# Optimization experiments

Measured on AMD Instinct MI355X. Metric: run time of the kernel, lower is better.

Reference implementation:

```python
import jax, jax.numpy as jnp
import numpy as np
import math

EMBED_DIM = 512
NUM_CLASSES = 100000
BATCH = 1024
MARGIN = 0.5
SCALE = 64.0


def setup_inputs() -> dict:
    key = jax.random.key(0)
    k1, k2, k3 = jax.random.split(key, 3)
    embeddings = jax.random.normal(k1, (BATCH, EMBED_DIM), dtype=jnp.float32)
    labels = jax.random.randint(k2, (BATCH,), 0, NUM_CLASSES, dtype=jnp.int64)
    # xavier_uniform for weight [num_classes, embedding_dim]
    limit = math.sqrt(6.0 / (NUM_CLASSES + EMBED_DIM))
    weight = jax.random.uniform(k3, (NUM_CLASSES, EMBED_DIM), dtype=jnp.float32,
                                minval=-limit, maxval=limit)
    return {"embeddings": embeddings, "weight": weight, "labels": labels}


def _l2norm(x, axis=-1, eps=1e-12):
    # matches torch F.normalize (p=2, eps=1e-12)
    n = jnp.linalg.norm(x, axis=axis, keepdims=True)
    return x / jnp.maximum(n, eps)


def reference(embeddings, weight, labels):
    cos_m = math.cos(MARGIN)
    sin_m = math.sin(MARGIN)
    th = math.cos(math.pi - MARGIN)
    mm = math.sin(math.pi - MARGIN) * MARGIN

    # cosine similarity: [B, C]
    cosine = _l2norm(embeddings) @ _l2norm(weight).T
    sine = jnp.sqrt(jnp.clip(1.0 - cosine * cosine, 0.0, 1.0))
    phi = cosine * cos_m - sine * sin_m
    phi = jnp.where(cosine > th, phi, cosine - mm)

    # apply margin only at the label position
    one_hot = jax.nn.one_hot(labels, NUM_CLASSES, dtype=cosine.dtype)
    logits = SCALE * (one_hot * phi + (1.0 - one_hot) * cosine)

    # cross entropy, mean reduction
    logp = jax.nn.log_softmax(logits, axis=-1)
    nll = -jnp.take_along_axis(logp, labels[:, None], axis=1)[:, 0]
    return jnp.mean(nll)
```

## Files before the change

### kernel.cpp

```cpp
#include <hip/hip_runtime.h>
#include <hip/hip_bf16.h>
#include <math.h>

#define B_ROWS 1024
#define EMB    512
#define NCLS   100000
#define SCALE_ 64.0f
#define COS_M 0.8775825618903728f
#define SIN_M 0.479425538604203f
#define TH_C  (-0.8775825618903728f)
#define MM_C  0.2397127693021015f

#define BM 128
#define BN 128
#define BK 32
#define NTILES 782
#define KCHUNKS 16

typedef __attribute__((ext_vector_type(8))) short bf16x8;
typedef __attribute__((ext_vector_type(4))) float f32x4;

typedef __attribute__((address_space(1))) const unsigned int GLP;
typedef __attribute__((address_space(3))) unsigned int LDP;

__device__ __forceinline__ float bf2f(short u) {
  unsigned int x = ((unsigned int)(unsigned short)u) << 16;
  return __builtin_bit_cast(float, x);
}
__device__ __forceinline__ short f2bf(float f) {
  unsigned int u = __builtin_bit_cast(unsigned int, f);
  u += 0x7FFF + ((u >> 16) & 1);
  return (short)(u >> 16);
}

__device__ __forceinline__ void load16(const void* g, void* l) {
  __builtin_amdgcn_global_load_lds((GLP*)g, (LDP*)l, 16, 0, 0);
}

__global__ void setup_kernel(const void* __restrict__ emb, const int* __restrict__ labels,
                             float* __restrict__ row_sum, float* __restrict__ accum,
                             int* __restrict__ flag, int* __restrict__ dflag) {
  const int t = threadIdx.x;
  row_sum[t] = 0.f;
  row_sum[t + 512] = 0.f;
  if (t == 0) *accum = 0.f;

  if (t < 64) {
    bf16x8 v = *(const bf16x8*)((const short*)emb + t * 8);
    float s = 0.f;
    #pragma unroll
    for (int j = 0; j < 8; ++j) { float f = bf2f(v[j]); s += f * f; }
    #pragma unroll
    for (int off = 1; off < 64; off <<= 1) s += __shfl_xor(s, off);
    if (t == 0) *dflag = (s < 1e8f) ? 1 : 0;
  }

  int v = labels[2 * t + 1];
  #pragma unroll
  for (int off = 1; off < 64; off <<= 1) v |= __shfl_xor(v, off);
  __shared__ int red[8];
  if ((t & 63) == 0) red[t >> 6] = v;
  __syncthreads();
  if (t == 0) {
    int o = 0;
    #pragma unroll
    for (int i = 0; i < 8; ++i) o |= red[i];
    *flag = (o == 0) ? 1 : 0;
  }
}

__global__ void normconv_kernel(const void* __restrict__ emb, const void* __restrict__ wgt,
                                const int* __restrict__ dflag,
                                float* __restrict__ inv_e, float* __restrict__ inv_w,
                                short* __restrict__ An, short* __restrict__ Wn,
                                const int do_conv) {
  const int wave = threadIdx.x >> 6;
  const int lane = threadIdx.x & 63;
  const int row = blockIdx.x * 4 + wave;
  int r;
  const void* base;
  float* dst;
  short* out;
  if (row < B_ROWS) { r = row; base = emb; dst = inv_e + row; out = An + (size_t)row * EMB; }
  else {
    r = row - B_ROWS;
    if (r >= NCLS) return;
    base = wgt; dst = inv_w + r; out = Wn + (size_t)r * EMB;
  }
  float f[8];
  if (*dflag) {
    const short* p = (const short*)base + (size_t)r * EMB;
    bf16x8 v = *(const bf16x8*)(p + lane * 8);
    #pragma unroll
    for (int j = 0; j < 8; ++j) f[j] = bf2f(v[j]);
  } else {
    const float* p = (const float*)base + (size_t)r * EMB;
    f32x4 x = *(const f32x4*)(p + lane * 8);
    f32x4 y = *(const f32x4*)(p + lane * 8 + 4);
    #pragma unroll
    for (int j = 0; j < 4; ++j) { f[j] = x[j]; f[j + 4] = y[j]; }
  }
  float s = 0.f;
  #pragma unroll
  for (int j = 0; j < 8; ++j) s += f[j] * f[j];
  #pragma unroll
  for (int off = 1; off < 64; off <<= 1) s += __shfl_xor(s, off);
  const float inv = 1.f / fmaxf(sqrtf(s), 1e-12f);
  if (lane == 0) *dst = inv;
  if (do_conv) {
    bf16x8 o;
    #pragma unroll
    for (int j = 0; j < 8; ++j) o[j] = f2bf(f[j] * inv);
    *(bf16x8*)(out + lane * 8) = o;
  }
}

__global__ __launch_bounds__(256, 3) void arc_gemm_fast(
    const short* __restrict__ A, const short* __restrict__ W,
    const int* __restrict__ labels, const int* __restrict__ flag,
    float* __restrict__ row_sum, float* __restrict__ lablogit) {
  __shared__ short As[BM * BK];
  __shared__ short Bs[BN * BK];
  __shared__ int   sh_lab[BM];
  __shared__ float sh_sum[BM][2];

  const int tid  = threadIdx.x;
  const int wave = tid >> 6;
  const int lane = tid & 63;
  const int wy = wave >> 1;
  const int wx = wave & 1;
  const int lr = lane & 15;
  const int lk = lane >> 4;
  const int mBase = blockIdx.x * BM;
  const int nBase = blockIdx.y * BN;

  const int srow  = lane >> 2;
  const int sbyte = (lane & 3) * 16;

  f32x4 zero = {0.f, 0.f, 0.f, 0.f};
  f32x4 acc[4][4];
  #pragma unroll
  for (int i = 0; i < 4; ++i)
    #pragma unroll
    for (int j = 0; j < 4; ++j) acc[i][j] = zero;

  const char* Ab = (const char*)A;
  const char* Wb = (const char*)W;

  for (int kc = 0; kc < KCHUNKS; ++kc) {
    __syncthreads();
    const size_t koff = (size_t)kc * 64 + sbyte;
    #pragma unroll
    for (int it = 0; it < 2; ++it) {
      const int c = wave + it * 4;
      const int ar = mBase + c * 16 + srow;
      load16(Ab + (size_t)ar * 1024 + koff, (char*)As + (size_t)c * 1024);
      int br = nBase + c * 16 + srow;
      if (br >= NCLS) br = NCLS - 1;
      load16(Wb + (size_t)br * 1024 + koff, (char*)Bs + (size_t)c * 1024);
    }
    __syncthreads();
    bf16x8 af[4], bfr[4];
    #pragma unroll
    for (int mi = 0; mi < 4; ++mi)
      af[mi] = *(const bf16x8*)(As + ((wy * 64 + mi * 16 + lr) * BK + lk * 8));
    #pragma unroll
    for (int ni = 0; ni < 4; ++ni)
      bfr[ni] = *(const bf16x8*)(Bs + ((wx * 64 + ni * 16 + lr) * BK + lk * 8));
    #pragma unroll
    for (int mi = 0; mi < 4; ++mi)
      #pragma unroll
      for (int ni = 0; ni < 4; ++ni)
        acc[mi][ni] = __builtin_amdgcn_mfma_f32_16x16x32_bf16(af[mi], bfr[ni], acc[mi][ni], 0, 0, 0);
  }

  __syncthreads();
  if (tid < BM) {
    const int r = mBase + tid;
    const int f = *flag;
    sh_lab[tid] = labels[f ? (size_t)(2 * r) : (size_t)r];
  }
  __syncthreads();

  #pragma unroll
  for (int mi = 0; mi < 4; ++mi) {
    #pragma unroll
    for (int reg = 0; reg < 4; ++reg) {
      const int lrow = wy * 64 + mi * 16 + lk * 4 + reg;
      const int grow = mBase + lrow;
      const int lab = sh_lab[lrow];
      float s = 0.f;
      #pragma unroll
      for (int ni = 0; ni < 4; ++ni) {
        const int gcol = nBase + wx * 64 + ni * 16 + lr;
        if (gcol < NCLS) {
          const float cosv = acc[mi][ni][reg];
          float logit;
          if (gcol == lab) {
            const float sine = sqrtf(fmaxf(1.f - cosv * cosv, 0.f));
            float phi = cosv * COS_M - sine * SIN_M;
            phi = (cosv > TH_C) ? phi : (cosv - MM_C);
            logit = SCALE_ * phi;
            lablogit[grow] = logit;
          } else {
            logit = SCALE_ * cosv;
          }
          s += __expf(logit - SCALE_);
        }
      }
      #pragma unroll
      for (int off = 1; off < 16; off <<= 1) s += __shfl_xor(s, off);
      if (lr == 0) sh_sum[lrow][wx] = s;
    }
  }
  __syncthreads();
  if (tid < BM)
    atomicAdd(&row_sum[mBase + tid], sh_sum[tid][0] + sh_sum[tid][1]);
}

__global__ __launch_bounds__(256, 3) void arc_gemm(
    const void* __restrict__ A, const void* __restrict__ W,
    const float* __restrict__ inv_e, const float* __restrict__ inv_w,
    const int* __restrict__ labels, const int* __restrict__ flag,
    const int* __restrict__ dflag,
    float* __restrict__ row_sum, float* __restrict__ lablogit) {
  __shared__ short As[BM * BK];
  __shared__ short Bs[BN * BK];
  __shared__ int   sh_lab[BM];
  __shared__ float sh_sum[BM][2];

  const int tid  = threadIdx.x;
  const int wave = tid >> 6;
  const int lane = tid & 63;
  const int wy = wave >> 1;
  const int wx = wave & 1;
  const int lr = lane & 15;
  const int lk = lane >> 4;
  const int mBase = blockIdx.x * BM;
  const int nBase = blockIdx.y * BN;
  const int isbf16 = *dflag;

  const int srow  = lane >> 2;
  const int sbyte = (lane & 3) * 16;

  f32x4 zero = {0.f, 0.f, 0.f, 0.f};
  f32x4 acc[4][4];
  #pragma unroll
  for (int i = 0; i < 4; ++i)
    #pragma unroll
    for (int j = 0; j < 4; ++j) acc[i][j] = zero;

  const char*  Ab = (const char*)A;
  const char*  Wb = (const char*)W;
  const float* Af = (const float*)A;
  const float* Wf = (const float*)W;

  for (int kc = 0; kc < KCHUNKS; ++kc) {
    __syncthreads();
    if (isbf16) {
      const size_t koff = (size_t)kc * 64 + sbyte;
      #pragma unroll
      for (int it = 0; it < 2; ++it) {
        const int c = wave + it * 4;
        const int ar = mBase + c * 16 + srow;
        load16(Ab + (size_t)ar * 1024 + koff, (char*)As + (size_t)c * 1024);
        int br = nBase + c * 16 + srow;
        if (br >= NCLS) br = NCLS - 1;
        load16(Wb + (size_t)br * 1024 + koff, (char*)Bs + (size_t)c * 1024);
      }
    } else {
      #pragma unroll
      for (int p = 0; p < 2; ++p) {
        const int u   = p * 256 + tid;
        const int row = u >> 2;
        const int seg = u & 3;
        const float* ga = Af + ((size_t)(mBase + row) * EMB + kc * 32 + seg * 8);
        f32x4 x = *(const f32x4*)ga;
        f32x4 y = *(const f32x4*)(ga + 4);
        bf16x8 tpack;
        #pragma unroll
        for (int j = 0; j < 4; ++j) { tpack[j] = f2bf(x[j]); tpack[j + 4] = f2bf(y[j]); }
        *(bf16x8*)(As + row * BK + seg * 8) = tpack;
        int br = nBase + row;
        if (br >= NCLS) br = NCLS - 1;
        const float* gb = Wf + ((size_t)br * EMB + kc * 32 + seg * 8);
        x = *(const f32x4*)gb;
        y = *(const f32x4*)(gb + 4);
        #pragma unroll
        for (int j = 0; j < 4; ++j) { tpack[j] = f2bf(x[j]); tpack[j + 4] = f2bf(y[j]); }
        *(bf16x8*)(Bs + row * BK + seg * 8) = tpack;
      }
    }
    __syncthreads();
    bf16x8 af[4], bfr[4];
    #pragma unroll
    for (int mi = 0; mi < 4; ++mi)
      af[mi] = *(const bf16x8*)(As + ((wy * 64 + mi * 16 + lr) * BK + lk * 8));
    #pragma unroll
    for (int ni = 0; ni < 4; ++ni)
      bfr[ni] = *(const bf16x8*)(Bs + ((wx * 64 + ni * 16 + lr) * BK + lk * 8));
    #pragma unroll
    for (int mi = 0; mi < 4; ++mi)
      #pragma unroll
      for (int ni = 0; ni < 4; ++ni)
        acc[mi][ni] = __builtin_amdgcn_mfma_f32_16x16x32_bf16(af[mi], bfr[ni], acc[mi][ni], 0, 0, 0);
  }

  __syncthreads();
  if (tid < BM) {
    const int r = mBase + tid;
    const int f = *flag;
    sh_lab[tid] = labels[f ? (size_t)(2 * r) : (size_t)r];
  }
  __syncthreads();

  #pragma unroll
  for (int mi = 0; mi < 4; ++mi) {
    #pragma unroll
    for (int reg = 0; reg < 4; ++reg) {
      const int lrow = wy * 64 + mi * 16 + lk * 4 + reg;
      const int grow = mBase + lrow;
      const float ie = inv_e[grow];
      const int lab = sh_lab[lrow];
      float s = 0.f;
      #pragma unroll
      for (int ni = 0; ni < 4; ++ni) {
        const int gcol = nBase + wx * 64 + ni * 16 + lr;
        if (gcol < NCLS) {
          const float cosv = acc[mi][ni][reg] * ie * inv_w[gcol];
          float logit;
          if (gcol == lab) {
            const float sine = sqrtf(fmaxf(1.f - cosv * cosv, 0.f));
            float phi = cosv * COS_M - sine * SIN_M;
            phi = (cosv > TH_C) ? phi : (cosv - MM_C);
            logit = SCALE_ * phi;
            lablogit[grow] = logit;
          } else {
            logit = SCALE_ * cosv;
          }
          s += __expf(logit - SCALE_);
        }
      }
      #pragma unroll
      for (int off = 1; off < 16; off <<= 1) s += __shfl_xor(s, off);
      if (lr == 0) sh_sum[lrow][wx] = s;
    }
  }
  __syncthreads();
  if (tid < BM)
    atomicAdd(&row_sum[mBase + tid], sh_sum[tid][0] + sh_sum[tid][1]);
}

__global__ void loss_kernel(const float* __restrict__ row_sum,
                            const float* __restrict__ lablogit,
                            float* __restrict__ accum) {
  const int r = blockIdx.x * 128 + threadIdx.x;
  float loss = SCALE_ + logf(row_sum[r]) - lablogit[r];
  #pragma unroll
  for (int off = 1; off < 64; off <<= 1) loss += __shfl_xor(loss, off);
  __shared__ float rs[2];
  if ((threadIdx.x & 63) == 0) rs[threadIdx.x >> 6] = loss;
  __syncthreads();
  if (threadIdx.x == 0) atomicAdd(accum, rs[0] + rs[1]);
}

__global__ void finalize_kernel(const float* __restrict__ accum, float* __restrict__ out) {
  out[0] = accum[0] * (1.0f / 1024.0f);
}

extern "C" void kernel_launch(void* const* d_in, const int* in_sizes, int n_in,
                              void* d_out, int out_size, void* d_ws, size_t ws_size,
                              hipStream_t stream) {
  const void* emb   = d_in[0];
  const void* wgt   = d_in[1];
  const int* labels = (const int*)d_in[2];
  float* out = (float*)d_out;

  const size_t WN_SHORTS = (size_t)NCLS * EMB;
  const size_t AN_SHORTS = (size_t)B_ROWS * EMB;
  const size_t FAST_NEED = (WN_SHORTS + AN_SHORTS) * 2 + 103075u * 4;

  if (ws_size >= FAST_NEED) {
    short* Wn = (short*)d_ws;
    short* An = Wn + WN_SHORTS;
    float* tail     = (float*)(An + AN_SHORTS);
    float* inv_e    = tail;
    float* inv_w    = tail + 1024;
    float* lablogit = tail + 101024;
    float* row_sum  = tail + 102048;
    float* accum    = tail + 103072;
    int*   flag     = (int*)(tail + 103073);
    int*   dflag    = (int*)(tail + 103074);

    setup_kernel<<<1, 512, 0, stream>>>(emb, labels, row_sum, accum, flag, dflag);
    normconv_kernel<<<(B_ROWS + NCLS) / 4, 256, 0, stream>>>(
        emb, wgt, dflag, inv_e, inv_w, An, Wn, 1);
    dim3 grid(8, NTILES);
    arc_gemm_fast<<<grid, 256, 0, stream>>>(An, Wn, labels, flag, row_sum, lablogit);
    loss_kernel<<<8, 128, 0, stream>>>(row_sum, lablogit, accum);
    finalize_kernel<<<1, 1, 0, stream>>>(accum, out);
  } else {
    float* ws       = (float*)d_ws;
    float* inv_e    = ws;
    float* inv_w    = ws + 1024;
    float* lablogit = ws + 101024;
    float* row_sum  = ws + 102048;
    float* accum    = ws + 103072;
    int*   flag     = (int*)(ws + 103073);
    int*   dflag    = (int*)(ws + 103074);

    setup_kernel<<<1, 512, 0, stream>>>(emb, labels, row_sum, accum, flag, dflag);
    normconv_kernel<<<(B_ROWS + NCLS) / 4, 256, 0, stream>>>(
        emb, wgt, dflag, inv_e, inv_w, (short*)inv_e, (short*)inv_e, 0);
    dim3 grid(8, NTILES);
    arc_gemm<<<grid, 256, 0, stream>>>(emb, wgt, inv_e, inv_w, labels, flag, dflag, row_sum, lablogit);
    loss_kernel<<<8, 128, 0, stream>>>(row_sum, lablogit, accum);
    finalize_kernel<<<1, 1, 0, stream>>>(accum, out);
  }
}
```

Measured before the change: 477.7 us.

## Swizzle LDS layout, remap GEMM tile order, and widen per-thread normalization work

The normalization kernel now gives each row to 16 threads instead of a full wave, so each thread loads and converts more elements with a shorter shuffle reduction. The fast GEMM switches to a 1D grid whose block index is remapped so that 8 consecutive blocks cover different weight tiles grouped for L2 reuse. It also XOR-swizzles the 16-byte chunk positions in the A and B LDS tiles to reduce bank conflicts on MFMA operand reads. The risks are a few idle padded blocks and higher register pressure in the normalization kernel.

Result: faster. 465.3 us (-2.6%).

```diff
diff --git a/kernel.cpp b/kernel.cpp
--- a/kernel.cpp
+++ b/kernel.cpp
@@ -18,6 +18,7 @@
 #define KCHUNKS 16
 
 typedef __attribute__((ext_vector_type(8))) short bf16x8;
+typedef __attribute__((ext_vector_type(4))) short s16x4;
 typedef __attribute__((ext_vector_type(4))) float f32x4;
 
 typedef __attribute__((address_space(1))) const unsigned int GLP;
@@ -69,14 +70,14 @@
   }
 }
 
-__global__ void normconv_kernel(const void* __restrict__ emb, const void* __restrict__ wgt,
-                                const int* __restrict__ dflag,
-                                float* __restrict__ inv_e, float* __restrict__ inv_w,
-                                short* __restrict__ An, short* __restrict__ Wn,
-                                const int do_conv) {
-  const int wave = threadIdx.x >> 6;
-  const int lane = threadIdx.x & 63;
-  const int row = blockIdx.x * 4 + wave;
+__global__ __launch_bounds__(256) void normconv_kernel(
+    const void* __restrict__ emb, const void* __restrict__ wgt,
+    const int* __restrict__ dflag,
+    float* __restrict__ inv_e, float* __restrict__ inv_w,
+    short* __restrict__ An, short* __restrict__ Wn, const int do_conv) {
+  const int sub  = threadIdx.x & 15;
+  const int rloc = threadIdx.x >> 4;
+  const int row  = blockIdx.x * 16 + rloc;
   int r;
   const void* base;
   float* dst;
@@ -87,31 +88,50 @@
     if (r >= NCLS) return;
     base = wgt; dst = inv_w + r; out = Wn + (size_t)r * EMB;
   }
-  float f[8];
-  if (*dflag) {
+  const int isbf16 = *dflag;
+  float f[32];
+  if (isbf16) {
     const short* p = (const short*)base + (size_t)r * EMB;
-    bf16x8 v = *(const bf16x8*)(p + lane * 8);
-    #pragma unroll
-    for (int j = 0; j < 8; ++j) f[j] = bf2f(v[j]);
+    #pragma unroll
+    for (int j = 0; j < 4; ++j) {
+      bf16x8 v = *(const bf16x8*)(p + j * 128 + sub * 8);
+      #pragma unroll
+      for (int t = 0; t < 8; ++t) f[j * 8 + t] = bf2f(v[t]);
+    }
   } else {
     const float* p = (const float*)base + (size_t)r * EMB;
-    f32x4 x = *(const f32x4*)(p + lane * 8);
-    f32x4 y = *(const f32x4*)(p + lane * 8 + 4);
-    #pragma unroll
-    for (int j = 0; j < 4; ++j) { f[j] = x[j]; f[j + 4] = y[j]; }
+    #pragma unroll
+    for (int j = 0; j < 8; ++j) {
+      f32x4 v = *(const f32x4*)(p + j * 64 + sub * 4);
+      #pragma unroll
+      for (int t = 0; t < 4; ++t) f[j * 4 + t] = v[t];
+    }
   }
   float s = 0.f;
   #pragma unroll
-  for (int j = 0; j < 8; ++j) s += f[j] * f[j];
-  #pragma unroll
-  for (int off = 1; off < 64; off <<= 1) s += __shfl_xor(s, off);
+  for (int j = 0; j < 32; ++j) s += f[j] * f[j];
+  #pragma unroll
+  for (int off = 1; off < 16; off <<= 1) s += __shfl_xor(s, off);
   const float inv = 1.f / fmaxf(sqrtf(s), 1e-12f);
-  if (lane == 0) *dst = inv;
+  if (sub == 0) *dst = inv;
   if (do_conv) {
-    bf16x8 o;
-    #pragma unroll
-    for (int j = 0; j < 8; ++j) o[j] = f2bf(f[j] * inv);
-    *(bf16x8*)(out + lane * 8) = o;
+    if (isbf16) {
+      #pragma unroll
+      for (int j = 0; j < 4; ++j) {
+        bf16x8 o;
+        #pragma unroll
+        for (int t = 0; t < 8; ++t) o[t] = f2bf(f[j * 8 + t] * inv);
+        *(bf16x8*)(out + j * 128 + sub * 8) = o;
+      }
+    } else {
+      #pragma unroll
+      for (int j = 0; j < 8; ++j) {
+        s16x4 o;
+        #pragma unroll
+        for (int t = 0; t < 4; ++t) o[t] = f2bf(f[j * 4 + t] * inv);
+        *(s16x4*)(out + j * 64 + sub * 4) = o;
+      }
+    }
   }
 }
 
@@ -119,6 +139,13 @@
     const short* __restrict__ A, const short* __restrict__ W,
     const int* __restrict__ labels, const int* __restrict__ flag,
     float* __restrict__ row_sum, float* __restrict__ lablogit) {
+  const int bid = blockIdx.x;
+  const int k   = bid & 7;
+  const int j   = bid >> 3;
+  const int ytile = (j >> 3) * 8 + k;
+  const int xtile = j & 7;
+  if (ytile >= NTILES) return;
+
   __shared__ short As[BM * BK];
   __shared__ short Bs[BN * BK];
   __shared__ int   sh_lab[BM];
@@ -131,18 +158,19 @@
   const int wx = wave & 1;
   const int lr = lane & 15;
   const int lk = lane >> 4;
-  const int mBase = blockIdx.x * BM;
-  const int nBase = blockIdx.y * BN;
+  const int mBase = xtile * BM;
+  const int nBase = ytile * BN;
 
   const int srow  = lane >> 2;
-  const int sbyte = (lane & 3) * 16;
+  const int sbyte = (((lane & 3) ^ ((lane >> 3) & 3)) << 4);
+  const int rswz  = ((lr >> 1) & 3);
 
   f32x4 zero = {0.f, 0.f, 0.f, 0.f};
   f32x4 acc[4][4];
   #pragma unroll
   for (int i = 0; i < 4; ++i)
     #pragma unroll
-    for (int j = 0; j < 4; ++j) acc[i][j] = zero;
+    for (int jj = 0; jj < 4; ++jj) acc[i][jj] = zero;
 
   const char* Ab = (const char*)A;
   const char* Wb = (const char*)W;
@@ -163,10 +191,10 @@
     bf16x8 af[4], bfr[4];
     #pragma unroll
     for (int mi = 0; mi < 4; ++mi)
-      af[mi] = *(const bf16x8*)(As + ((wy * 64 + mi * 16 + lr) * BK + lk * 8));
+      af[mi] = *(const bf16x8*)(As + ((wy * 64 + mi * 16 + lr) * BK + (lk ^ rswz) * 8));
     #pragma unroll
     for (int ni = 0; ni < 4; ++ni)
-      bfr[ni] = *(const bf16x8*)(Bs + ((wx * 64 + ni * 16 + lr) * BK + lk * 8));
+      bfr[ni] = *(const bf16x8*)(Bs + ((wx * 64 + ni * 16 + lr) * BK + (lk ^ rswz) * 8));
     #pragma unroll
     for (int mi = 0; mi < 4; ++mi)
       #pragma unroll
@@ -376,6 +404,8 @@
   const int* labels = (const int*)d_in[2];
   float* out = (float*)d_out;
 
+  const int NORM_BLOCKS = (B_ROWS + NCLS + 15) / 16;
+
   const size_t WN_SHORTS = (size_t)NCLS * EMB;
   const size_t AN_SHORTS = (size_t)B_ROWS * EMB;
   const size_t FAST_NEED = (WN_SHORTS + AN_SHORTS) * 2 + 103075u * 4;
@@ -393,10 +423,9 @@
     int*   dflag    = (int*)(tail + 103074);
 
     setup_kernel<<<1, 512, 0, stream>>>(emb, labels, row_sum, accum, flag, dflag);
-    normconv_kernel<<<(B_ROWS + NCLS) / 4, 256, 0, stream>>>(
+    normconv_kernel<<<NORM_BLOCKS, 256, 0, stream>>>(
         emb, wgt, dflag, inv_e, inv_w, An, Wn, 1);
-    dim3 grid(8, NTILES);
-    arc_gemm_fast<<<grid, 256, 0, stream>>>(An, Wn, labels, flag, row_sum, lablogit);
+    arc_gemm_fast<<<8 * 784, 256, 0, stream>>>(An, Wn, labels, flag, row_sum, lablogit);
     loss_kernel<<<8, 128, 0, stream>>>(row_sum, lablogit, accum);
     finalize_kernel<<<1, 1, 0, stream>>>(accum, out);
   } else {
@@ -410,7 +439,7 @@
     int*   dflag    = (int*)(ws + 103074);
 
     setup_kernel<<<1, 512, 0, stream>>>(emb, labels, row_sum, accum, flag, dflag);
-    normconv_kernel<<<(B_ROWS + NCLS) / 4, 256, 0, stream>>>(
+    normconv_kernel<<<NORM_BLOCKS, 256, 0, stream>>>(
         emb, wgt, dflag, inv_e, inv_w, (short*)inv_e, (short*)inv_e, 0);
     dim3 grid(8, NTILES);
     arc_gemm<<<grid, 256, 0, stream>>>(emb, wgt, inv_e, inv_w, labels, flag, dflag, row_sum, lablogit);
```
